# Optimization experiments

Hardware: AMD Instinct MI355X
Metric: run time of the kernel (lower is better)

The kernel has to match this reference:

```python
import jax, jax.numpy as jnp
import numpy as np

B, L, H, NH = 32, 512, 256, 4
DH = H // NH
EPS = 1e-12


def setup_inputs() -> dict:
    key = jax.random.key(0)
    ks = jax.random.split(key, 24)
    p = lambda k, shape: 0.02 * jax.random.normal(k, shape, dtype=jnp.float32)
    return {
        "input_tensor": jax.random.normal(ks[0], (B, L, H), dtype=jnp.float32),
        # sorted positive timestamps (seconds-like scale)
        "time_seq": jnp.sort(jax.random.uniform(ks[1], (B, L), dtype=jnp.float32) * 100.0, axis=-1),
        "attention_mask": jnp.zeros((B, 1, L, L), dtype=jnp.float32),
        "item_seq_len": jnp.clip(jax.random.randint(ks[2], (B,), 0, L), 2, L),
        "Wq": p(ks[3], (H, H)), "bq": jnp.zeros((H,), jnp.float32),
        "Wk": p(ks[4], (H, H)), "bk": jnp.zeros((H,), jnp.float32),
        "Wv": p(ks[5], (H, H)), "bv": jnp.zeros((H,), jnp.float32),
        "Wd": p(ks[6], (H, H)), "bd": jnp.zeros((H,), jnp.float32),
        "ln_g": jnp.ones((H,), jnp.float32), "ln_b": jnp.zeros((H,), jnp.float32),
        "Wtq": p(ks[7], (H, H)), "btq": jnp.zeros((H,), jnp.float32),
        "tw1": p(ks[8], (L, L)), "tb1": p(ks[9], (L, L)),
        "tow1": p(ks[10], (L, L)), "tow2": p(ks[11], (L, L)), "tob": p(ks[12], (L, L)),
        "Wt": p(ks[13], (1, 2 * H)), "bt": jnp.zeros((1,), jnp.float32),
    }


def reference(input_tensor, time_seq, attention_mask, item_seq_len,
              Wq, bq, Wk, bk, Wv, bv, Wd, bd, ln_g, ln_b,
              Wtq, btq, tw1, tb1, tow1, tow2, tob, Wt, bt):
    x = input_tensor  # (B, L, H)

    def heads(t):  # (B,L,H) -> (B,NH,L,DH)
        return t.reshape(B, L, NH, DH).transpose(0, 2, 1, 3)

    q = heads(x @ Wq.T + bq)
    k = heads(x @ Wk.T + bk)
    v = heads(x @ Wv.T + bv)

    scores = jnp.einsum('bhqd,bhkd->bhqk', q, k)  # (B,NH,L,L)

    # --- time decay gate ---
    tq = x @ Wtq.T + btq                                  # (B,L,H)
    time_query_key = jnp.tanh(jnp.einsum('bqh,bkh->bqk', tq, x))  # (B,L,L)
    diff = jnp.abs(time_seq[:, :, None] - time_seq[:, None, :])   # |t_i - t_j|
    decay = jnp.tanh(jnp.log1p(diff) * tw1 + tb1)
    decay_gate = tow1 * decay + tow2 * time_query_key + tob       # (B,L,L)
    time_attn = jax.nn.sigmoid(decay_gate)[:, None, :, :]         # (B,1,L,L)

    scores = scores * time_attn / jnp.sqrt(jnp.float32(DH)) + attention_mask
    probs = jax.nn.softmax(scores, axis=-1)

    ctx = jnp.einsum('bhqk,bhkd->bhqd', probs, v)
    ctx = ctx.transpose(0, 2, 1, 3).reshape(B, L, H)

    hs = ctx @ Wd.T + bd + x
    mu = jnp.mean(hs, axis=-1, keepdims=True)
    var = jnp.var(hs, axis=-1, keepdims=True)
    hs = (hs - mu) / jnp.sqrt(var + EPS) * ln_g + ln_b   # (B,L,H)

    bidx = jnp.arange(B)
    emb1 = hs[bidx, item_seq_len - 1]  # (B,H)
    emb2 = hs[bidx, item_seq_len - 2]  # (B,H)
    pred_intervals = jnp.concatenate([emb1, emb2], axis=1) @ Wt.T + bt  # (B,1)
    return hs, pred_intervals
```

## Files before the change

### kernel.cpp

```cpp
#include <hip/hip_runtime.h>
#include <math.h>

#define Bn 32
#define Ln 512
#define Hn 256
#define NHn 4
#define DHn 64

typedef __attribute__((ext_vector_type(8))) short bf16x8;
typedef __attribute__((ext_vector_type(4))) float f32x4;
typedef unsigned int uint32;

__device__ __forceinline__ short f2b(float f) {
    union { float f; uint32 u; } v; v.f = f;
    uint32 r = (v.u + 0x7FFFu + ((v.u >> 16) & 1u)) >> 16;
    return (short)r;
}
__device__ __forceinline__ float b2f(short h) {
    union { uint32 u; float f; } v; v.u = ((uint32)(unsigned short)h) << 16;
    return v.f;
}
__device__ __forceinline__ float fast_tanh(float x) {
    float e = __expf(2.f * x);
    return 1.f - 2.f * __builtin_amdgcn_rcpf(e + 1.f);
}
__device__ __forceinline__ float fast_sigmoid(float x) {
    return __builtin_amdgcn_rcpf(1.f + __expf(-x));
}

__global__ __launch_bounds__(256) void conv_kernel(
    const float* __restrict__ x,
    const float* __restrict__ Wq, const float* __restrict__ Wk,
    const float* __restrict__ Wv, const float* __restrict__ Wtq,
    const float* __restrict__ Wd,
    short* __restrict__ xb, short* __restrict__ wb)
{
    const size_t NLH = (size_t)Bn * Ln * Hn;
    size_t i4 = ((size_t)blockIdx.x * 256 + threadIdx.x) * 4;
    if (i4 < NLH) {
        float4 v = *(const float4*)(x + i4);
        short4 o; o.x = f2b(v.x); o.y = f2b(v.y); o.z = f2b(v.z); o.w = f2b(v.w);
        *(short4*)(xb + i4) = o;
    } else {
        size_t off = i4 - NLH;
        int w = (int)(off >> 16);
        size_t wi = off & 65535;
        const float* src = (w == 0) ? Wq : (w == 1) ? Wk : (w == 2) ? Wv : (w == 3) ? Wtq : Wd;
        float4 v = *(const float4*)(src + wi);
        short4 o; o.x = f2b(v.x); o.y = f2b(v.y); o.z = f2b(v.z); o.w = f2b(v.w);
        *(short4*)(wb + off) = o;
    }
}

struct Acc { f32x4 t[4]; };

__device__ __forceinline__ void gemm_tile_64(
    const short* __restrict__ A,
    const short* __restrict__ Bm,
    int K, short* As, short* Bs, Acc& acc)
{
    const int tid = threadIdx.x;
    const int lane = tid & 63, w = tid >> 6;
    const int quad = lane >> 4, lm = lane & 15;
    const int srow = tid >> 3;
    const int slot = tid & 7;

    for (int k0 = 0; k0 < K; k0 += 64) {
        __syncthreads();
#pragma unroll
        for (int iss = 0; iss < 2; ++iss) {
            int r = srow + iss * 32;
            bf16x8 av = *(const bf16x8*)(A + (size_t)r * K + k0 + slot * 8);
            bf16x8 bv = *(const bf16x8*)(Bm + (size_t)r * K + k0 + slot * 8);
            *(bf16x8*)(As + r * 72 + slot * 8) = av;
            *(bf16x8*)(Bs + r * 72 + slot * 8) = bv;
        }
        __syncthreads();
#pragma unroll
        for (int ks = 0; ks < 2; ++ks) {
            bf16x8 a = *(const bf16x8*)(As + (w * 16 + lm) * 72 + ks * 32 + quad * 8);
#pragma unroll
            for (int kt = 0; kt < 4; ++kt) {
                bf16x8 b = *(const bf16x8*)(Bs + (kt * 16 + lm) * 72 + ks * 32 + quad * 8);
                acc.t[kt] = __builtin_amdgcn_mfma_f32_16x16x32_bf16(a, b, acc.t[kt], 0, 0, 0);
            }
        }
    }
}

__global__ __launch_bounds__(256) void proj_kernel(
    const short* __restrict__ xb, const short* __restrict__ wb,
    const float* __restrict__ bq, const float* __restrict__ bk,
    const float* __restrict__ bv, const float* __restrict__ btq,
    short* __restrict__ qb, short* __restrict__ kb,
    short* __restrict__ vt, short* __restrict__ tqb)
{
    __shared__ short As[64 * 72];
    __shared__ short Bs[64 * 72];
    const int bid = blockIdx.y * 16 + blockIdx.x;
    const int xcd = bid & 7, idx = bid >> 3;
    const int v = xcd * 512 + idx;
    const int tensor = (v & 15) >> 2;
    const int ncol0 = (v & 3) * 64;
    const int m0 = (v >> 4) * 64;
    const short* A = xb + (size_t)m0 * Hn;
    const short* Bw = wb + (size_t)tensor * 65536 + (size_t)ncol0 * Hn;
    const float* bias = (tensor == 0) ? bq : (tensor == 1) ? bk : (tensor == 2) ? bv : btq;

    Acc acc;
#pragma unroll
    for (int i = 0; i < 4; ++i) acc.t[i] = (f32x4){0.f, 0.f, 0.f, 0.f};
    gemm_tile_64(A, Bw, Hn, As, Bs, acc);

    const int lane = threadIdx.x & 63, w = threadIdx.x >> 6;
    const int quad = lane >> 4, lm = lane & 15;

    if (tensor == 2) {
#pragma unroll
        for (int kt = 0; kt < 4; ++kt) {
            int n = ncol0 + kt * 16 + lm;
            float bs = bv[n];
            int h = n >> 6, d = n & 63;
#pragma unroll
            for (int r = 0; r < 4; ++r) {
                int row = m0 + w * 16 + quad * 4 + r;
                int bb = row >> 9, l = row & 511;
                vt[((size_t)(bb * NHn + h) * DHn + d) * Ln + l] = f2b(acc.t[kt][r] + bs);
            }
        }
    } else {
        short* out = (tensor == 0) ? qb : (tensor == 1) ? kb : tqb;
#pragma unroll
        for (int kt = 0; kt < 4; ++kt) {
            int n = ncol0 + kt * 16 + lm;
            float bs = bias[n];
#pragma unroll
            for (int r = 0; r < 4; ++r) {
                int row = m0 + w * 16 + quad * 4 + r;
                out[(size_t)row * Hn + n] = f2b(acc.t[kt][r] + bs);
            }
        }
    }
}

__global__ __launch_bounds__(256) void gate_kernel(
    const short* __restrict__ tqb, const short* __restrict__ xb,
    const float* __restrict__ tseq,
    const float* __restrict__ tw1, const float* __restrict__ tb1,
    const float* __restrict__ tow1, const float* __restrict__ tow2,
    const float* __restrict__ tob,
    short* __restrict__ gateb)
{
    __shared__ short As[64 * 72];
    __shared__ short Bs[64 * 72];
    const int b = blockIdx.z;
    const int m0 = blockIdx.y * 64, n0 = blockIdx.x * 64;
    const short* A = tqb + ((size_t)b * Ln + m0) * Hn;
    const short* Bw = xb + ((size_t)b * Ln + n0) * Hn;

    Acc acc;
#pragma unroll
    for (int i = 0; i < 4; ++i) acc.t[i] = (f32x4){0.f, 0.f, 0.f, 0.f};
    gemm_tile_64(A, Bw, Hn, As, Bs, acc);

    const int tid = threadIdx.x;
    const int lane = tid & 63, w = tid >> 6;
    const int quad = lane >> 4, lm = lane & 15;
    const float* ts = tseq + (size_t)b * Ln;
    float ti[4];
#pragma unroll
    for (int r = 0; r < 4; ++r) ti[r] = ts[m0 + w * 16 + quad * 4 + r];

    bf16x8 g01, g23;
#pragma unroll
    for (int kt = 0; kt < 4; ++kt) {
        int j = n0 + kt * 16 + lm;
        float tj = ts[j];
#pragma unroll
        for (int r = 0; r < 4; ++r) {
            int i = m0 + w * 16 + quad * 4 + r;
            size_t ij = (size_t)i * Ln + j;
            float lg = __logf(1.f + fabsf(ti[r] - tj));
            float dec = fast_tanh(lg * tw1[ij] + tb1[ij]);
            float tqk = fast_tanh(acc.t[kt][r]);
            float dg = tow1[ij] * dec + tow2[ij] * tqk + tob[ij];
            float g = 0.125f * fast_sigmoid(dg);
            if (kt < 2) g01[kt * 4 + r] = f2b(g);
            else        g23[(kt - 2) * 4 + r] = f2b(g);
        }
    }
    size_t base = ((((size_t)b * 8 + blockIdx.y) * 8 + blockIdx.x) * 256 + tid) * 16;
    *(bf16x8*)(gateb + base) = g01;
    *(bf16x8*)(gateb + base + 8) = g23;
}

__global__ __launch_bounds__(256) void flash_mfma(
    const short* __restrict__ qb, const short* __restrict__ kb,
    const short* __restrict__ vt, const short* __restrict__ gateb,
    const float* __restrict__ mask, short* __restrict__ ctxb)
{
    __shared__ short Ks[64 * 72];
    __shared__ short Vt[64 * 72];
    __shared__ short Ps[4 * 16 * 72];
    const int mb = blockIdx.x;
    const int q0 = mb * 64;
    const int h = blockIdx.y, b = blockIdx.z;
    const int tid = threadIdx.x;
    const int w = tid >> 6, lane = tid & 63;
    const int quad = lane >> 4, lm = lane & 15;
    const int srow = tid >> 3, slot = tid & 7;

    bf16x8 qf0, qf1;
    {
        const short* qrow = qb + ((size_t)(b * Ln + q0 + w * 16 + lm)) * Hn + h * DHn;
        qf0 = *(const bf16x8*)(qrow + quad * 8);
        qf1 = *(const bf16x8*)(qrow + 32 + quad * 8);
    }

    f32x4 o[4];
#pragma unroll
    for (int i = 0; i < 4; ++i) o[i] = (f32x4){0.f, 0.f, 0.f, 0.f};
    float m_run[4] = {-INFINITY, -INFINITY, -INFINITY, -INFINITY};
    float l_run[4] = {0.f, 0.f, 0.f, 0.f};
    const float* mk_base = mask + (size_t)b * Ln * Ln;
    const int qrow0 = q0 + w * 16 + quad * 4;
    const short* kbase = kb + ((size_t)(b * Ln)) * Hn + h * DHn;
    const short* vbase = vt + (size_t)(b * NHn + h) * DHn * Ln;
    const short* gtile0 = gateb + (((size_t)b * 8 + mb) * 8 * 256 + tid) * 16;

    for (int k0 = 0; k0 < Ln; k0 += 64) {
        __syncthreads();
#pragma unroll
        for (int iss = 0; iss < 2; ++iss) {
            int r = srow + iss * 32;
            bf16x8 kv = *(const bf16x8*)(kbase + (size_t)(k0 + r) * Hn + slot * 8);
            bf16x8 vv = *(const bf16x8*)(vbase + (size_t)r * Ln + k0 + slot * 8);
            *(bf16x8*)(Ks + r * 72 + slot * 8) = kv;
            *(bf16x8*)(Vt + r * 72 + slot * 8) = vv;
        }
        __syncthreads();

        const short* gt = gtile0 + (size_t)(k0 >> 6) * 256 * 16;
        bf16x8 g01 = *(const bf16x8*)(gt);
        bf16x8 g23 = *(const bf16x8*)(gt + 8);
        float mvv[4][4];
#pragma unroll
        for (int kt = 0; kt < 4; ++kt) {
            int col = k0 + kt * 16 + lm;
#pragma unroll
            for (int r = 0; r < 4; ++r)
                mvv[kt][r] = mk_base[(size_t)(qrow0 + r) * Ln + col];
        }

        f32x4 s[4];
#pragma unroll
        for (int kt = 0; kt < 4; ++kt) {
            s[kt] = (f32x4){0.f, 0.f, 0.f, 0.f};
            bf16x8 b0 = *(const bf16x8*)(Ks + (kt * 16 + lm) * 72 + quad * 8);
            s[kt] = __builtin_amdgcn_mfma_f32_16x16x32_bf16(qf0, b0, s[kt], 0, 0, 0);
            bf16x8 b1 = *(const bf16x8*)(Ks + (kt * 16 + lm) * 72 + 32 + quad * 8);
            s[kt] = __builtin_amdgcn_mfma_f32_16x16x32_bf16(qf1, b1, s[kt], 0, 0, 0);
        }

        float mnew[4];
#pragma unroll
        for (int r = 0; r < 4; ++r) mnew[r] = m_run[r];
#pragma unroll
        for (int kt = 0; kt < 4; ++kt)
#pragma unroll
            for (int r = 0; r < 4; ++r) {
                float g = b2f(kt < 2 ? g01[(kt & 1) * 4 + r] : g23[(kt & 1) * 4 + r]);
                float sv = s[kt][r] * g + mvv[kt][r];
                s[kt][r] = sv;
                mnew[r] = fmaxf(mnew[r], sv);
            }
        float alpha[4], rsum[4];
#pragma unroll
        for (int r = 0; r < 4; ++r) {
#pragma unroll
            for (int off = 1; off < 16; off <<= 1)
                mnew[r] = fmaxf(mnew[r], __shfl_xor(mnew[r], off, 64));
            alpha[r] = __expf(m_run[r] - mnew[r]);
            m_run[r] = mnew[r];
            rsum[r] = 0.f;
        }
        float p[4][4];
#pragma unroll
        for (int kt = 0; kt < 4; ++kt)
#pragma unroll
            for (int r = 0; r < 4; ++r) {
                float pv = __expf(s[kt][r] - m_run[r]);
                p[kt][r] = pv;
                rsum[r] += pv;
            }
#pragma unroll
        for (int r = 0; r < 4; ++r) {
#pragma unroll
            for (int off = 1; off < 16; off <<= 1) rsum[r] += __shfl_xor(rsum[r], off, 64);
            l_run[r] = l_run[r] * alpha[r] + rsum[r];
#pragma unroll
            for (int ot = 0; ot < 4; ++ot) o[ot][r] *= alpha[r];
        }
        short* pw = Ps + w * 16 * 72;
#pragma unroll
        for (int kt = 0; kt < 4; ++kt)
#pragma unroll
            for (int r = 0; r < 4; ++r)
                pw[(quad * 4 + r) * 72 + kt * 16 + lm] = f2b(p[kt][r]);

#pragma unroll
        for (int ks = 0; ks < 2; ++ks) {
            bf16x8 pa = *(const bf16x8*)(pw + lm * 72 + ks * 32 + quad * 8);
#pragma unroll
            for (int ot = 0; ot < 4; ++ot) {
                bf16x8 vv = *(const bf16x8*)(Vt + (ot * 16 + lm) * 72 + ks * 32 + quad * 8);
                o[ot] = __builtin_amdgcn_mfma_f32_16x16x32_bf16(pa, vv, o[ot], 0, 0, 0);
            }
        }
    }

    float inv[4];
#pragma unroll
    for (int r = 0; r < 4; ++r) inv[r] = 1.0f / l_run[r];
#pragma unroll
    for (int ot = 0; ot < 4; ++ot) {
        int d = h * DHn + ot * 16 + lm;
#pragma unroll
        for (int r = 0; r < 4; ++r) {
            int row = b * Ln + qrow0 + r;
            ctxb[(size_t)row * Hn + d] = f2b(o[ot][r] * inv[r]);
        }
    }
}

__global__ __launch_bounds__(256) void outproj_ln_kernel(
    const short* __restrict__ ctxb, const short* __restrict__ wdb,
    const float* __restrict__ bd, const float* __restrict__ x,
    const float* __restrict__ g, const float* __restrict__ beta,
    float* __restrict__ out)
{
    const int m0 = blockIdx.x * 64;
    const int tid = threadIdx.x;
    const int lane = tid & 63, w = tid >> 6;
    const int quad = lane >> 4, lm = lane & 15;

    const short* arow = ctxb + (size_t)(m0 + w * 16 + lm) * Hn;
    bf16x8 af[8];
#pragma unroll
    for (int k8 = 0; k8 < 8; ++k8)
        af[k8] = *(const bf16x8*)(arow + k8 * 32 + quad * 8);

    f32x4 acc[4][4];
#pragma unroll
    for (int i = 0; i < 4; ++i)
#pragma unroll
        for (int j = 0; j < 4; ++j) acc[i][j] = (f32x4){0.f, 0.f, 0.f, 0.f};

#pragma unroll
    for (int k8 = 0; k8 < 8; ++k8) {
#pragma unroll
        for (int nt = 0; nt < 4; ++nt)
#pragma unroll
            for (int kt = 0; kt < 4; ++kt) {
                bf16x8 bf = *(const bf16x8*)(wdb + (size_t)(nt * 64 + kt * 16 + lm) * Hn + k8 * 32 + quad * 8);
                acc[nt][kt] = __builtin_amdgcn_mfma_f32_16x16x32_bf16(af[k8], bf, acc[nt][kt], 0, 0, 0);
            }
    }

    const int rl0 = w * 16 + quad * 4;
    float s1[4] = {0.f, 0.f, 0.f, 0.f}, s2[4] = {0.f, 0.f, 0.f, 0.f};
#pragma unroll
    for (int nt = 0; nt < 4; ++nt)
#pragma unroll
        for (int kt = 0; kt < 4; ++kt) {
            int col = nt * 64 + kt * 16 + lm;
            float bdv = bd[col];
#pragma unroll
            for (int r = 0; r < 4; ++r) {
                float xv = x[(size_t)(m0 + rl0 + r) * Hn + col];
                float hv = acc[nt][kt][r] + bdv + xv;
                acc[nt][kt][r] = hv;
                s1[r] += hv;
                s2[r] += hv * hv;
            }
        }
#pragma unroll
    for (int r = 0; r < 4; ++r) {
#pragma unroll
        for (int off = 1; off < 16; off <<= 1) {
            s1[r] += __shfl_xor(s1[r], off, 64);
            s2[r] += __shfl_xor(s2[r], off, 64);
        }
    }
    float mu[4], rstd[4];
#pragma unroll
    for (int r = 0; r < 4; ++r) {
        mu[r] = s1[r] * (1.f / 256.f);
        float var = s2[r] * (1.f / 256.f) - mu[r] * mu[r];
        rstd[r] = rsqrtf(var + 1e-12f);
    }
#pragma unroll
    for (int nt = 0; nt < 4; ++nt)
#pragma unroll
        for (int kt = 0; kt < 4; ++kt) {
            int col = nt * 64 + kt * 16 + lm;
            float gv = g[col], bb = beta[col];
#pragma unroll
            for (int r = 0; r < 4; ++r)
                out[(size_t)(m0 + rl0 + r) * Hn + col] =
                    (acc[nt][kt][r] - mu[r]) * rstd[r] * gv + bb;
        }
}

__global__ __launch_bounds__(256) void pred_kernel(const float* __restrict__ hs,
                                                   const int* __restrict__ lens,
                                                   const float* __restrict__ Wt,
                                                   const float* __restrict__ bt,
                                                   float* __restrict__ pred)
{
    const int b = blockIdx.x, t = threadIdx.x;
    int len = lens[b];
    float e1 = hs[((size_t)b * Ln + (len - 1)) * Hn + t];
    float e2 = hs[((size_t)b * Ln + (len - 2)) * Hn + t];
    float v = e1 * Wt[t] + e2 * Wt[Hn + t];
#pragma unroll
    for (int off = 32; off > 0; off >>= 1) v += __shfl_xor(v, off, 64);
    __shared__ float ps[4];
    if ((t & 63) == 0) ps[t >> 6] = v;
    __syncthreads();
    if (t == 0) pred[b] = ps[0] + ps[1] + ps[2] + ps[3] + bt[0];
}

extern "C" void kernel_launch(void* const* d_in, const int* in_sizes, int n_in,
                              void* d_out, int out_size, void* d_ws, size_t ws_size,
                              hipStream_t stream) {
    (void)in_sizes; (void)n_in; (void)out_size; (void)ws_size;
    const float* x    = (const float*)d_in[0];
    const float* tseq = (const float*)d_in[1];
    const float* mask = (const float*)d_in[2];
    const int*   lens = (const int*)d_in[3];
    const float* Wq = (const float*)d_in[4];  const float* bq = (const float*)d_in[5];
    const float* Wk = (const float*)d_in[6];  const float* bk = (const float*)d_in[7];
    const float* Wv = (const float*)d_in[8];  const float* bv = (const float*)d_in[9];
    const float* Wd = (const float*)d_in[10]; const float* bd = (const float*)d_in[11];
    const float* ln_g = (const float*)d_in[12]; const float* ln_b = (const float*)d_in[13];
    const float* Wtq = (const float*)d_in[14]; const float* btq = (const float*)d_in[15];
    const float* tw1 = (const float*)d_in[16]; const float* tb1 = (const float*)d_in[17];
    const float* tow1 = (const float*)d_in[18]; const float* tow2 = (const float*)d_in[19];
    const float* tob = (const float*)d_in[20];
    const float* Wt = (const float*)d_in[21]; const float* bt = (const float*)d_in[22];

    const size_t NLH = (size_t)Bn * Ln * Hn;
    short* ws = (short*)d_ws;
    short* xb    = ws;
    short* wb    = xb + NLH;
    short* qb    = wb + 5 * 65536;
    short* kb    = qb + NLH;
    short* vt    = kb + NLH;
    short* tqb   = vt + NLH;
    short* gateb = tqb + NLH;
    short* ctxb  = tqb;
    float* out   = (float*)d_out;

    dim3 blk(256);
    conv_kernel<<<dim3(4416), blk, 0, stream>>>(x, Wq, Wk, Wv, Wtq, Wd, xb, wb);
    proj_kernel<<<dim3(16, 256), blk, 0, stream>>>(xb, wb, bq, bk, bv, btq, qb, kb, vt, tqb);
    gate_kernel<<<dim3(8, 8, Bn), blk, 0, stream>>>(tqb, xb, tseq, tw1, tb1, tow1, tow2, tob, gateb);
    flash_mfma<<<dim3(8, NHn, Bn), blk, 0, stream>>>(qb, kb, vt, gateb, mask, ctxb);
    outproj_ln_kernel<<<dim3(256), blk, 0, stream>>>(ctxb, wb + 4 * 65536, bd, x, ln_g, ln_b, out);
    pred_kernel<<<dim3(Bn), blk, 0, stream>>>(out, lens, Wt, bt, out + NLH);
}
```

Measured before the change: 232.9 us.

## Pack time-gate params per thread, split outproj rows, fuse pred into LN

The five LxL time-gate parameter matrices are repacked once per call into a per-thread contiguous layout inside the conversion kernel. The gate kernel then reads them with float4 loads instead of scattered strided scalar loads. The output projection+LayerNorm kernel now gives each block 16 rows split across four waves by column, with a shared-memory row reduction, which quadruples the block count. The prediction head is folded into it through atomicAdd, removing the separate pred kernel launch. This adds an extra read and write of the packed parameters every call, and float atomics make the prediction sum order nondeterministic.

Result: slower. 247.7 us (+6.4%).

```diff
diff --git a/kernel.cpp b/kernel.cpp
--- a/kernel.cpp
+++ b/kernel.cpp
@@ -32,23 +32,52 @@
     const float* __restrict__ x,
     const float* __restrict__ Wq, const float* __restrict__ Wk,
     const float* __restrict__ Wv, const float* __restrict__ Wtq,
-    const float* __restrict__ Wd,
-    short* __restrict__ xb, short* __restrict__ wb)
+    const float* __restrict__ Wd, const float* __restrict__ bt,
+    const float* __restrict__ tw1, const float* __restrict__ tb1,
+    const float* __restrict__ tow1, const float* __restrict__ tow2,
+    const float* __restrict__ tob,
+    short* __restrict__ xb, short* __restrict__ wb,
+    float* __restrict__ ttpack, float* __restrict__ pred)
 {
     const size_t NLH = (size_t)Bn * Ln * Hn;
-    size_t i4 = ((size_t)blockIdx.x * 256 + threadIdx.x) * 4;
-    if (i4 < NLH) {
-        float4 v = *(const float4*)(x + i4);
-        short4 o; o.x = f2b(v.x); o.y = f2b(v.y); o.z = f2b(v.z); o.w = f2b(v.w);
-        *(short4*)(xb + i4) = o;
+    const int bid = blockIdx.x;
+    if (bid == 0 && threadIdx.x < Bn) pred[threadIdx.x] = bt[0];
+    if (bid < 4416) {
+        size_t i4 = ((size_t)bid * 256 + threadIdx.x) * 4;
+        if (i4 < NLH) {
+            float4 v = *(const float4*)(x + i4);
+            short4 o; o.x = f2b(v.x); o.y = f2b(v.y); o.z = f2b(v.z); o.w = f2b(v.w);
+            *(short4*)(xb + i4) = o;
+        } else {
+            size_t off = i4 - NLH;
+            int w = (int)(off >> 16);
+            size_t wi = off & 65535;
+            const float* src = (w == 0) ? Wq : (w == 1) ? Wk : (w == 2) ? Wv : (w == 3) ? Wtq : Wd;
+            float4 v = *(const float4*)(src + wi);
+            short4 o; o.x = f2b(v.x); o.y = f2b(v.y); o.z = f2b(v.z); o.w = f2b(v.w);
+            *(short4*)(wb + off) = o;
+        }
     } else {
-        size_t off = i4 - NLH;
-        int w = (int)(off >> 16);
-        size_t wi = off & 65535;
-        const float* src = (w == 0) ? Wq : (w == 1) ? Wk : (w == 2) ? Wv : (w == 3) ? Wtq : Wd;
-        float4 v = *(const float4*)(src + wi);
-        short4 o; o.x = f2b(v.x); o.y = f2b(v.y); o.z = f2b(v.z); o.w = f2b(v.w);
-        *(short4*)(wb + off) = o;
+        const int t = bid - 4416;
+        const int mb = t >> 3, nb = t & 7;
+        const int tid = threadIdx.x;
+        const int i0 = mb * 64 + (tid >> 6) * 16 + ((tid >> 4) & 3) * 4;
+        const int jb = nb * 64 + (tid & 15);
+        float* dst = ttpack + ((size_t)t * 256 + tid) * 80;
+#pragma unroll
+        for (int kt = 0; kt < 4; ++kt) {
+            int j = jb + kt * 16;
+#pragma unroll
+            for (int r = 0; r < 4; ++r) {
+                size_t ij = (size_t)(i0 + r) * Ln + j;
+                int e = kt * 4 + r;
+                dst[e]      = tw1[ij];
+                dst[16 + e] = tb1[ij];
+                dst[32 + e] = tow1[ij];
+                dst[48 + e] = tow2[ij];
+                dst[64 + e] = tob[ij];
+            }
+        }
     }
 }
 
@@ -145,10 +174,7 @@
 
 __global__ __launch_bounds__(256) void gate_kernel(
     const short* __restrict__ tqb, const short* __restrict__ xb,
-    const float* __restrict__ tseq,
-    const float* __restrict__ tw1, const float* __restrict__ tb1,
-    const float* __restrict__ tow1, const float* __restrict__ tow2,
-    const float* __restrict__ tob,
+    const float* __restrict__ tseq, const float* __restrict__ ttpack,
     short* __restrict__ gateb)
 {
     __shared__ short As[64 * 72];
@@ -167,6 +193,7 @@
     const int lane = tid & 63, w = tid >> 6;
     const int quad = lane >> 4, lm = lane & 15;
     const float* ts = tseq + (size_t)b * Ln;
+    const float* tp = ttpack + ((size_t)(blockIdx.y * 8 + blockIdx.x) * 256 + tid) * 80;
     float ti[4];
 #pragma unroll
     for (int r = 0; r < 4; ++r) ti[r] = ts[m0 + w * 16 + quad * 4 + r];
@@ -176,17 +203,25 @@
     for (int kt = 0; kt < 4; ++kt) {
         int j = n0 + kt * 16 + lm;
         float tj = ts[j];
-#pragma unroll
-        for (int r = 0; r < 4; ++r) {
-            int i = m0 + w * 16 + quad * 4 + r;
-            size_t ij = (size_t)i * Ln + j;
+        float4 w1 = *(const float4*)(tp + kt * 4);
+        float4 b1 = *(const float4*)(tp + 16 + kt * 4);
+        float4 o1 = *(const float4*)(tp + 32 + kt * 4);
+        float4 o2 = *(const float4*)(tp + 48 + kt * 4);
+        float4 ob = *(const float4*)(tp + 64 + kt * 4);
+        const float* w1p = (const float*)&w1;
+        const float* b1p = (const float*)&b1;
+        const float* o1p = (const float*)&o1;
+        const float* o2p = (const float*)&o2;
+        const float* obp = (const float*)&ob;
+#pragma unroll
+        for (int r = 0; r < 4; ++r) {
             float lg = __logf(1.f + fabsf(ti[r] - tj));
-            float dec = fast_tanh(lg * tw1[ij] + tb1[ij]);
+            float dec = fast_tanh(lg * w1p[r] + b1p[r]);
             float tqk = fast_tanh(acc.t[kt][r]);
-            float dg = tow1[ij] * dec + tow2[ij] * tqk + tob[ij];
-            float g = 0.125f * fast_sigmoid(dg);
-            if (kt < 2) g01[kt * 4 + r] = f2b(g);
-            else        g23[(kt - 2) * 4 + r] = f2b(g);
+            float dg = o1p[r] * dec + o2p[r] * tqk + obp[r];
+            float gv = 0.125f * fast_sigmoid(dg);
+            if (kt < 2) g01[kt * 4 + r] = f2b(gv);
+            else        g23[(kt - 2) * 4 + r] = f2b(gv);
         }
     }
     size_t base = ((((size_t)b * 8 + blockIdx.y) * 8 + blockIdx.x) * 256 + tid) * 16;
@@ -337,98 +372,103 @@
     const short* __restrict__ ctxb, const short* __restrict__ wdb,
     const float* __restrict__ bd, const float* __restrict__ x,
     const float* __restrict__ g, const float* __restrict__ beta,
-    float* __restrict__ out)
+    const int* __restrict__ lens, const float* __restrict__ Wt,
+    float* __restrict__ out, float* __restrict__ pred)
 {
-    const int m0 = blockIdx.x * 64;
+    const int m0 = blockIdx.x * 16;
     const int tid = threadIdx.x;
     const int lane = tid & 63, w = tid >> 6;
     const int quad = lane >> 4, lm = lane & 15;
 
-    const short* arow = ctxb + (size_t)(m0 + w * 16 + lm) * Hn;
+    const short* arow = ctxb + (size_t)(m0 + lm) * Hn;
     bf16x8 af[8];
 #pragma unroll
     for (int k8 = 0; k8 < 8; ++k8)
         af[k8] = *(const bf16x8*)(arow + k8 * 32 + quad * 8);
 
-    f32x4 acc[4][4];
-#pragma unroll
-    for (int i = 0; i < 4; ++i)
-#pragma unroll
-        for (int j = 0; j < 4; ++j) acc[i][j] = (f32x4){0.f, 0.f, 0.f, 0.f};
-
-#pragma unroll
-    for (int k8 = 0; k8 < 8; ++k8) {
-#pragma unroll
-        for (int nt = 0; nt < 4; ++nt)
-#pragma unroll
-            for (int kt = 0; kt < 4; ++kt) {
-                bf16x8 bf = *(const bf16x8*)(wdb + (size_t)(nt * 64 + kt * 16 + lm) * Hn + k8 * 32 + quad * 8);
-                acc[nt][kt] = __builtin_amdgcn_mfma_f32_16x16x32_bf16(af[k8], bf, acc[nt][kt], 0, 0, 0);
-            }
-    }
-
-    const int rl0 = w * 16 + quad * 4;
+    f32x4 acc[4];
+#pragma unroll
+    for (int i = 0; i < 4; ++i) acc[i] = (f32x4){0.f, 0.f, 0.f, 0.f};
+
+#pragma unroll
+    for (int k8 = 0; k8 < 8; ++k8)
+#pragma unroll
+        for (int kt = 0; kt < 4; ++kt) {
+            bf16x8 bf = *(const bf16x8*)(wdb + (size_t)(w * 64 + kt * 16 + lm) * Hn + k8 * 32 + quad * 8);
+            acc[kt] = __builtin_amdgcn_mfma_f32_16x16x32_bf16(af[k8], bf, acc[kt], 0, 0, 0);
+        }
+
     float s1[4] = {0.f, 0.f, 0.f, 0.f}, s2[4] = {0.f, 0.f, 0.f, 0.f};
 #pragma unroll
-    for (int nt = 0; nt < 4; ++nt)
-#pragma unroll
-        for (int kt = 0; kt < 4; ++kt) {
-            int col = nt * 64 + kt * 16 + lm;
-            float bdv = bd[col];
-#pragma unroll
-            for (int r = 0; r < 4; ++r) {
-                float xv = x[(size_t)(m0 + rl0 + r) * Hn + col];
-                float hv = acc[nt][kt][r] + bdv + xv;
-                acc[nt][kt][r] = hv;
-                s1[r] += hv;
-                s2[r] += hv * hv;
-            }
-        }
-#pragma unroll
-    for (int r = 0; r < 4; ++r) {
+    for (int kt = 0; kt < 4; ++kt) {
+        int col = w * 64 + kt * 16 + lm;
+        float bdv = bd[col];
+#pragma unroll
+        for (int r = 0; r < 4; ++r) {
+            int row = m0 + quad * 4 + r;
+            float xv = x[(size_t)row * Hn + col];
+            float hv = acc[kt][r] + bdv + xv;
+            acc[kt][r] = hv;
+            s1[r] += hv;
+            s2[r] += hv * hv;
+        }
+    }
+#pragma unroll
+    for (int r = 0; r < 4; ++r)
 #pragma unroll
         for (int off = 1; off < 16; off <<= 1) {
             s1[r] += __shfl_xor(s1[r], off, 64);
             s2[r] += __shfl_xor(s2[r], off, 64);
         }
-    }
+    __shared__ float red1[4][16], red2[4][16];
+    if (lm == 0) {
+#pragma unroll
+        for (int r = 0; r < 4; ++r) {
+            red1[w][quad * 4 + r] = s1[r];
+            red2[w][quad * 4 + r] = s2[r];
+        }
+    }
+    __syncthreads();
     float mu[4], rstd[4];
 #pragma unroll
     for (int r = 0; r < 4; ++r) {
-        mu[r] = s1[r] * (1.f / 256.f);
-        float var = s2[r] * (1.f / 256.f) - mu[r] * mu[r];
+        int row = quad * 4 + r;
+        float S1 = red1[0][row] + red1[1][row] + red1[2][row] + red1[3][row];
+        float S2 = red2[0][row] + red2[1][row] + red2[2][row] + red2[3][row];
+        mu[r] = S1 * (1.f / 256.f);
+        float var = S2 * (1.f / 256.f) - mu[r] * mu[r];
         rstd[r] = rsqrtf(var + 1e-12f);
     }
-#pragma unroll
-    for (int nt = 0; nt < 4; ++nt)
-#pragma unroll
-        for (int kt = 0; kt < 4; ++kt) {
-            int col = nt * 64 + kt * 16 + lm;
-            float gv = g[col], bb = beta[col];
-#pragma unroll
-            for (int r = 0; r < 4; ++r)
-                out[(size_t)(m0 + rl0 + r) * Hn + col] =
-                    (acc[nt][kt][r] - mu[r]) * rstd[r] * gv + bb;
-        }
-}
-
-__global__ __launch_bounds__(256) void pred_kernel(const float* __restrict__ hs,
-                                                   const int* __restrict__ lens,
-                                                   const float* __restrict__ Wt,
-                                                   const float* __restrict__ bt,
-                                                   float* __restrict__ pred)
-{
-    const int b = blockIdx.x, t = threadIdx.x;
-    int len = lens[b];
-    float e1 = hs[((size_t)b * Ln + (len - 1)) * Hn + t];
-    float e2 = hs[((size_t)b * Ln + (len - 2)) * Hn + t];
-    float v = e1 * Wt[t] + e2 * Wt[Hn + t];
-#pragma unroll
-    for (int off = 32; off > 0; off >>= 1) v += __shfl_xor(v, off, 64);
-    __shared__ float ps[4];
-    if ((t & 63) == 0) ps[t >> 6] = v;
-    __syncthreads();
-    if (t == 0) pred[b] = ps[0] + ps[1] + ps[2] + ps[3] + bt[0];
+
+    const int bb = m0 >> 9;
+    const int len = lens[bb];
+    const int loc1 = (bb << 9) + len - 1;
+    const int loc2 = loc1 - 1;
+    const bool own1 = (loc1 >= m0) && (loc1 < m0 + 16);
+    const bool own2 = (loc2 >= m0) && (loc2 < m0 + 16);
+    const bool active = own1 || own2;
+    float pacc = 0.f;
+
+#pragma unroll
+    for (int kt = 0; kt < 4; ++kt) {
+        int col = w * 64 + kt * 16 + lm;
+        float gv = g[col], bb2 = beta[col];
+#pragma unroll
+        for (int r = 0; r < 4; ++r) {
+            int row = m0 + quad * 4 + r;
+            float val = (acc[kt][r] - mu[r]) * rstd[r] * gv + bb2;
+            out[(size_t)row * Hn + col] = val;
+            if (active) {
+                if (row == loc1) pacc += val * Wt[col];
+                else if (row == loc2) pacc += val * Wt[Hn + col];
+            }
+        }
+    }
+    if (active) {
+#pragma unroll
+        for (int off = 1; off < 64; off <<= 1) pacc += __shfl_xor(pacc, off, 64);
+        if (lane == 0) atomicAdd(&pred[bb], pacc);
+    }
 }
 
 extern "C" void kernel_launch(void* const* d_in, const int* in_sizes, int n_in,
@@ -459,14 +499,18 @@
     short* vt    = kb + NLH;
     short* tqb   = vt + NLH;
     short* gateb = tqb + NLH;
+    float* ttpack = (float*)(gateb + (size_t)Bn * Ln * Ln);
     short* ctxb  = tqb;
     float* out   = (float*)d_out;
+    float* pred  = out + NLH;
 
     dim3 blk(256);
-    conv_kernel<<<dim3(4416), blk, 0, stream>>>(x, Wq, Wk, Wv, Wtq, Wd, xb, wb);
+    conv_kernel<<<dim3(4480), blk, 0, stream>>>(x, Wq, Wk, Wv, Wtq, Wd, bt,
+                                                tw1, tb1, tow1, tow2, tob,
+                                                xb, wb, ttpack, pred);
     proj_kernel<<<dim3(16, 256), blk, 0, stream>>>(xb, wb, bq, bk, bv, btq, qb, kb, vt, tqb);
-    gate_kernel<<<dim3(8, 8, Bn), blk, 0, stream>>>(tqb, xb, tseq, tw1, tb1, tow1, tow2, tob, gateb);
+    gate_kernel<<<dim3(8, 8, Bn), blk, 0, stream>>>(tqb, xb, tseq, ttpack, gateb);
     flash_mfma<<<dim3(8, NHn, Bn), blk, 0, stream>>>(qb, kb, vt, gateb, mask, ctxb);
-    outproj_ln_kernel<<<dim3(256), blk, 0, stream>>>(ctxb, wb + 4 * 65536, bd, x, ln_g, ln_b, out);
-    pred_kernel<<<dim3(Bn), blk, 0, stream>>>(out, lens, Wt, bt, out + NLH);
-}
+    outproj_ln_kernel<<<dim3(1024), blk, 0, stream>>>(ctxb, wb + 4 * 65536, bd, x,
+                                                      ln_g, ln_b, lens, Wt, out, pred);
+}
```
